# Kernel tuning notes

Measured on AMD Instinct MI355X. Metric: run time of the kernel, lower is better.

Reference implementation:

```python
import jax, jax.numpy as jnp
import numpy as np

N, H, C, G = 50000, 16, 8, 128   # nodes, heads, per-head channels, graphs
F_IN, NUM_CLASSES = 128, 2
E = 800000
HC = H * C
NEG_SLOPE = 0.2
BN_EPS = 1e-5


def setup_inputs() -> dict:
    key = jax.random.key(0)
    ks = jax.random.split(key, 32)
    s = 0.1
    p = lambda k, shape: (jax.random.normal(k, shape, jnp.float32) * s)
    inp = {
        "x": jax.random.normal(ks[0], (N, F_IN), jnp.float32),
        "edge_index": jax.random.randint(ks[1], (2, E), 0, N, dtype=jnp.int32),
        "batch": jnp.sort(jax.random.randint(ks[2], (N,), 0, G, dtype=jnp.int32)),
        # GAT layer 1 (in=F_IN)
        "W1": p(ks[3], (F_IN, HC)), "b1": p(ks[4], (HC,)),
        "asrc1": p(ks[5], (H, C)), "adst1": p(ks[6], (H, C)),
        "g1": 1.0 + p(ks[7], (HC,)), "beta1": p(ks[8], (HC,)),
        # GAT layer 2 (in=HC)
        "W2": p(ks[9], (HC, HC)), "b2": p(ks[10], (HC,)),
        "asrc2": p(ks[11], (H, C)), "adst2": p(ks[12], (H, C)),
        "g2": 1.0 + p(ks[13], (HC,)), "beta2": p(ks[14], (HC,)),
        # GAT layer 3
        "W3": p(ks[15], (HC, HC)), "b3": p(ks[16], (HC,)),
        "asrc3": p(ks[17], (H, C)), "adst3": p(ks[18], (H, C)),
        "g3": 1.0 + p(ks[19], (HC,)), "beta3": p(ks[20], (HC,)),
        # final linear + bn4
        "Wl": p(ks[21], (2 * HC, NUM_CLASSES)), "bl": p(ks[22], (NUM_CLASSES,)),
        "g4": 1.0 + p(ks[23], (NUM_CLASSES,)), "beta4": p(ks[24], (NUM_CLASSES,)),
    }
    return inp


def _gat(x, src, dst, W, b, asrc, adst):
    # x: [N, F_in] -> h: [N, H, C]
    h = (x @ W).reshape(N, H, C)
    a_s = jnp.einsum("nhc,hc->nh", h, asrc)  # [N,H]
    a_d = jnp.einsum("nhc,hc->nh", h, adst)
    e = jax.nn.leaky_relu(a_s[src] + a_d[dst], NEG_SLOPE)  # [E',H]
    # per-destination softmax (every node has a self loop -> segments non-empty)
    e_max = jax.ops.segment_max(e, dst, num_segments=N)
    ex = jnp.exp(e - e_max[dst])
    denom = jax.ops.segment_sum(ex, dst, num_segments=N)
    alpha = ex / (denom[dst] + 1e-16)  # [E',H]
    out = jax.ops.segment_sum(h[src] * alpha[:, :, None], dst, num_segments=N)
    return out.reshape(N, HC) + b


def _bn(x, g, beta):
    mu = jnp.mean(x, axis=0)
    var = jnp.mean((x - mu) ** 2, axis=0)  # biased, training-mode BN
    return (x - mu) * jax.lax.rsqrt(var + BN_EPS) * g + beta


def reference(x, edge_index, batch,
              W1, b1, asrc1, adst1, g1, beta1,
              W2, b2, asrc2, adst2, g2, beta2,
              W3, b3, asrc3, adst3, g3, beta3,
              Wl, bl, g4, beta4):
    # add self loops once (add_self_loops=True in every GATConv)
    loop = jnp.arange(N, dtype=edge_index.dtype)
    src = jnp.concatenate([edge_index[0], loop])
    dst = jnp.concatenate([edge_index[1], loop])

    h = jax.nn.relu(_bn(_gat(x, src, dst, W1, b1, asrc1, adst1), g1, beta1))
    h = jax.nn.relu(_bn(_gat(h, src, dst, W2, b2, asrc2, adst2), g2, beta2))
    h = jax.nn.relu(_bn(_gat(h, src, dst, W3, b3, asrc3, adst3), g3, beta3))

    pooled_sum = jax.ops.segment_sum(h, batch, num_segments=G)        # [G,HC]
    cnt = jax.ops.segment_sum(jnp.ones((N,), h.dtype), batch, num_segments=G)
    pooled_mean = pooled_sum / jnp.maximum(cnt, 1.0)[:, None]
    z = jnp.concatenate([pooled_mean, pooled_sum], axis=1)            # [G,2*HC]
    z = z @ Wl + bl
    return _bn(z, g4, beta4)
```

## Files before the change

kernel.cpp:

```cpp
#include <hip/hip_runtime.h>

#define NN 50000
#define NHEADS 16
#define NGRAPH 128
#define NEDGE 800000
#define NEP (NEDGE + NN)

#define EPB 2048
#define NBLK 416
#define NBUK 391
#define CASTB 3125
#define WTB 192
#define WASB 48

typedef float4 f4;
typedef __attribute__((ext_vector_type(4))) float f32x4;
typedef __attribute__((ext_vector_type(8))) short s8;

__device__ inline unsigned short f2b(float f) {
  union { float f; unsigned u; } v; v.f = f;
  unsigned r = v.u + 0x7FFFu + ((v.u >> 16) & 1u);
  return (unsigned short)(r >> 16);
}
__device__ inline float b2f(unsigned u16) {
  union { unsigned u; float f; } v; v.u = u16 << 16;
  return v.f;
}
__device__ inline float blo(unsigned u) {
  union { unsigned u; float f; } v; v.u = u << 16;
  return v.f;
}
__device__ inline float bhi(unsigned u) {
  union { unsigned u; float f; } v; v.u = u & 0xffff0000u;
  return v.f;
}


__global__ __launch_bounds__(256) void k_front(const int* __restrict__ ei, int* __restrict__ cntmat,
                                               const float* __restrict__ X, unsigned short* __restrict__ Xb,
                                               const float* __restrict__ W0, const float* __restrict__ W1, const float* __restrict__ W2,
                                               const float* __restrict__ as0, const float* __restrict__ as1, const float* __restrict__ as2,
                                               const float* __restrict__ ad0, const float* __restrict__ ad1, const float* __restrict__ ad2,
                                               unsigned short* __restrict__ T0, unsigned short* __restrict__ T1, unsigned short* __restrict__ T2,
                                               const int* __restrict__ batch, int* __restrict__ gstart) {
  __shared__ int hist[NBUK];
  int b = blockIdx.x, t = threadIdx.x;
  if (b < NBLK) {
    for (int k = t; k < NBUK; k += 256) hist[k] = 0;
    __syncthreads();
    int i0 = b * EPB;
    int i1 = i0 + EPB < NEP ? i0 + EPB : NEP;
    for (int i = i0 + t; i < i1; i += 256) {
      int d = (i < NEDGE) ? ei[NEDGE + i] : (i - NEDGE);
      atomicAdd(&hist[d >> 7], 1);
    }
    __syncthreads();
    for (int k = t; k < NBUK; k += 256) cntmat[b * NBUK + k] = hist[k];
    return;
  }
  int pb = b - NBLK;
  if (pb < CASTB) {
    int i = pb * 256 + t;
    const f4* X4 = (const f4*)X;
    f4 a = X4[2 * i], c = X4[2 * i + 1];
    uint4 o;
    o.x = (unsigned)f2b(a.x) | ((unsigned)f2b(a.y) << 16);
    o.y = (unsigned)f2b(a.z) | ((unsigned)f2b(a.w) << 16);
    o.z = (unsigned)f2b(c.x) | ((unsigned)f2b(c.y) << 16);
    o.w = (unsigned)f2b(c.z) | ((unsigned)f2b(c.w) << 16);
    ((uint4*)Xb)[i] = o;
  } else if (pb < CASTB + WTB) {
    int idx = (pb - CASTB) * 256 + t;
    int L = idx >> 14, r = idx & 16383;
    int n = r >> 7, kk = r & 127;
    const float* W = (L == 0) ? W0 : (L == 1) ? W1 : W2;
    unsigned short* T = (L == 0) ? T0 : (L == 1) ? T1 : T2;
    T[n * 128 + kk] = f2b(W[kk * 128 + n]);
  } else if (pb < CASTB + WTB + WASB) {
    int idx = (pb - CASTB - WTB) * 256 + t;
    int L = idx >> 12, r = idx & 4095;
    int h2 = r >> 7, kk = r & 127;
    int h = h2 & 15;
    const float* W = (L == 0) ? W0 : (L == 1) ? W1 : W2;
    const float* av = (h2 < 16) ? ((L == 0) ? as0 : (L == 1) ? as1 : as2)
                                : ((L == 0) ? ad0 : (L == 1) ? ad1 : ad2);
    unsigned short* T = (L == 0) ? T0 : (L == 1) ? T1 : T2;
    float s = 0.f;
#pragma unroll
    for (int c = 0; c < 8; ++c) s += W[kk * 128 + h * 8 + c] * av[h * 8 + c];
    T[(128 + h2) * 128 + kk] = f2b(s);
  } else {
    int g = t;
    if (g > NGRAPH) return;
    int lo = 0, hi = NN;
    while (lo < hi) { int mid = (lo + hi) >> 1; if (batch[mid] < g) lo = mid + 1; else hi = mid; }
    gstart[g] = lo;
  }
}


__global__ __launch_bounds__(512) void k_bscan(int* __restrict__ cntmat, int* __restrict__ btotal) {
  __shared__ int buf[512];
  int t = threadIdx.x, k = blockIdx.x;
  int v = (t < NBLK) ? cntmat[t * NBUK + k] : 0;
  buf[t] = v;
  __syncthreads();
  for (int off = 1; off < 512; off <<= 1) {
    int y = (t >= off) ? buf[t - off] : 0;
    __syncthreads();
    buf[t] += y;
    __syncthreads();
  }
  if (t < NBLK) cntmat[t * NBUK + k] = buf[t] - v;
  if (t == 511) btotal[k] = buf[511];
}

__global__ __launch_bounds__(512) void k_bbase(const int* __restrict__ btotal, int* __restrict__ bbase) {
  __shared__ int buf[512];
  int t = threadIdx.x;
  int v = (t < NBUK) ? btotal[t] : 0;
  buf[t] = v;
  __syncthreads();
  for (int off = 1; off < 512; off <<= 1) {
    int y = (t >= off) ? buf[t - off] : 0;
    __syncthreads();
    buf[t] += y;
    __syncthreads();
  }
  if (t < NBUK) bbase[t] = buf[t] - v;
  if (t == 511) bbase[NBUK] = buf[511];
}

__global__ __launch_bounds__(256) void k_bscatter(const int* __restrict__ ei, const int* __restrict__ cntmat,
                                                  const int* __restrict__ bbase, unsigned* __restrict__ pairs) {
  __shared__ int cur[NBUK];
  int t = threadIdx.x, b = blockIdx.x;
  for (int k = t; k < NBUK; k += 256) cur[k] = bbase[k] + cntmat[b * NBUK + k];
  __syncthreads();
  int i0 = b * EPB;
  int i1 = i0 + EPB < NEP ? i0 + EPB : NEP;
  for (int i = i0 + t; i < i1; i += 256) {
    int s, d;
    if (i < NEDGE) { s = ei[i]; d = ei[NEDGE + i]; }
    else { s = d = i - NEDGE; }
    int pos = atomicAdd(&cur[d >> 7], 1);
    pairs[pos] = ((unsigned)(d & 127) << 16) | (unsigned)s;
  }
}

__global__ __launch_bounds__(256) void k_bfinal(const unsigned* __restrict__ pairs, const int* __restrict__ bbase,
                                                int* __restrict__ row_off, int* __restrict__ colp) {
  __shared__ int cnt[128];
  __shared__ int buf[128];
  __shared__ int cur[128];
  int t = threadIdx.x, k = blockIdx.x;
  int n0 = k << 7;
  if (t < 128) cnt[t] = 0;
  __syncthreads();
  int p0 = bbase[k], p1 = bbase[k + 1];
  for (int i = p0 + t; i < p1; i += 256) atomicAdd(&cnt[pairs[i] >> 16], 1);
  __syncthreads();
  if (t < 128) buf[t] = cnt[t];
  __syncthreads();
  for (int off = 1; off < 128; off <<= 1) {
    int y = (t < 128 && t >= off) ? buf[t - off] : 0;
    __syncthreads();
    if (t < 128) buf[t] += y;
    __syncthreads();
  }
  if (t < 128) {
    int excl = buf[t] - cnt[t];
    cur[t] = p0 + excl;
    if (n0 + t < NN) row_off[n0 + t] = p0 + excl;
  }
  if (k == NBUK - 1 && t == 0) row_off[NN] = p1;
  __syncthreads();
  for (int i = p0 + t; i < p1; i += 256) {
    unsigned r = pairs[i];
    int pos = atomicAdd(&cur[r >> 16], 1);
    colp[pos] = (int)(r & 0xffffu);
  }
}


template<int FUSE>
__global__ __launch_bounds__(256) void k_gemm_t(const unsigned short* __restrict__ A, const unsigned short* __restrict__ Wt,
                                                const float* __restrict__ sc, unsigned short* __restrict__ Hb,
                                                unsigned short* __restrict__ Asb, float* __restrict__ Ad) {
  int w = threadIdx.x >> 6, l = threadIdx.x & 63;
  int r0 = blockIdx.x * 128 + w * 32;
  int lr = l & 15, lg = l >> 4;
  f32x4 acc[2][10];
#pragma unroll
  for (int m = 0; m < 2; ++m)
#pragma unroll
    for (int n = 0; n < 10; ++n) acc[m][n] = (f32x4){0.f, 0.f, 0.f, 0.f};

#pragma unroll
  for (int ks = 0; ks < 4; ++ks) {
    int koff = ks * 32 + lg * 8;
    s8 a[2];
    if constexpr (FUSE) {
      f4 s0 = *(const f4*)(sc + koff),       s1 = *(const f4*)(sc + koff + 4);
      f4 h0 = *(const f4*)(sc + 128 + koff), h1 = *(const f4*)(sc + 128 + koff + 4);
#pragma unroll
      for (int m = 0; m < 2; ++m) {
        int row = r0 + m * 16 + lr;
        row = (row < NN) ? row : (NN - 1);
        uint4 raw = *(const uint4*)(A + (size_t)row * 128 + koff);
        float v0 = fmaxf(blo(raw.x) * s0.x + h0.x, 0.f);
        float v1 = fmaxf(bhi(raw.x) * s0.y + h0.y, 0.f);
        float v2 = fmaxf(blo(raw.y) * s0.z + h0.z, 0.f);
        float v3 = fmaxf(bhi(raw.y) * s0.w + h0.w, 0.f);
        float v4 = fmaxf(blo(raw.z) * s1.x + h1.x, 0.f);
        float v5 = fmaxf(bhi(raw.z) * s1.y + h1.y, 0.f);
        float v6 = fmaxf(blo(raw.w) * s1.z + h1.z, 0.f);
        float v7 = fmaxf(bhi(raw.w) * s1.w + h1.w, 0.f);
        union { s8 v; uint4 u; } pk;
        pk.u.x = (unsigned)f2b(v0) | ((unsigned)f2b(v1) << 16);
        pk.u.y = (unsigned)f2b(v2) | ((unsigned)f2b(v3) << 16);
        pk.u.z = (unsigned)f2b(v4) | ((unsigned)f2b(v5) << 16);
        pk.u.w = (unsigned)f2b(v6) | ((unsigned)f2b(v7) << 16);
        a[m] = pk.v;
      }
    } else {
#pragma unroll
      for (int m = 0; m < 2; ++m) {
        int row = r0 + m * 16 + lr;
        row = (row < NN) ? row : (NN - 1);
        a[m] = *(const s8*)(A + (size_t)row * 128 + koff);
      }
    }
#pragma unroll
    for (int n = 0; n < 10; ++n) {
      s8 b = *(const s8*)(Wt + (size_t)(n * 16 + lr) * 128 + koff);
#pragma unroll
      for (int m = 0; m < 2; ++m)
        acc[m][n] = __builtin_amdgcn_mfma_f32_16x16x32_bf16(a[m], b, acc[m][n], 0, 0, 0);
    }
  }

#pragma unroll
  for (int m = 0; m < 2; ++m) {
    int rowb = r0 + m * 16 + lg * 4;
#pragma unroll
    for (int n = 0; n < 8; ++n) {
      int colb = n * 16 + lr;
#pragma unroll
      for (int reg = 0; reg < 4; ++reg) {
        int row = rowb + reg;
        if (row < NN) Hb[(size_t)row * 128 + colb] = f2b(acc[m][n][reg]);
      }
    }
#pragma unroll
    for (int reg = 0; reg < 4; ++reg) {
      int row = rowb + reg;
      if (row < NN) {
        Asb[row * 16 + lr] = f2b(acc[m][8][reg]);
        Ad[row * 16 + lr] = acc[m][9][reg];
      }
    }
  }
}


__global__ __launch_bounds__(256, 4) void k_agg(const unsigned short* __restrict__ Hb, const unsigned short* __restrict__ Asb,
                                                const float* __restrict__ Ad,
                                                const int* __restrict__ row_off, const int* __restrict__ col,
                                                unsigned short* __restrict__ Vb) {
  int b = blockIdx.x;
  int half = (b >> 2) & 1;
  int nb = (b >> 3) * 4 + (b & 3);
  if (nb >= 3125) return;
  int t = threadIdx.x;
  int node = nb * 16 + (t >> 4);
  int l = t & 15;
  int h = half * 8 + (l & 7);
  int par = l >> 3;
  int e0 = row_off[node], e1 = row_off[node + 1];
  float adh = Ad[node * 16 + h];
  float den = 0.f;
  float acc[8] = {0.f, 0.f, 0.f, 0.f, 0.f, 0.f, 0.f, 0.f};
  int j = e0 + par;
  for (; j + 14 < e1; j += 16) {
    int s[8];
#pragma unroll
    for (int q = 0; q < 8; ++q) s[q] = col[j + 2 * q];
    float a[8];
#pragma unroll
    for (int q = 0; q < 8; ++q) a[q] = b2f(Asb[s[q] * 16 + h]);
    uint4 p[8];
#pragma unroll
    for (int q = 0; q < 8; ++q) p[q] = *(const uint4*)(Hb + (size_t)s[q] * 128 + h * 8);
#pragma unroll
    for (int q = 0; q < 8; ++q) {
      float e = a[q] + adh;
      e = (e > 0.f) ? e : 0.2f * e;
      a[q] = __expf(e);
      den += a[q];
    }
#pragma unroll
    for (int q = 0; q < 8; ++q) {
      acc[0] += a[q] * blo(p[q].x); acc[1] += a[q] * bhi(p[q].x);
      acc[2] += a[q] * blo(p[q].y); acc[3] += a[q] * bhi(p[q].y);
      acc[4] += a[q] * blo(p[q].z); acc[5] += a[q] * bhi(p[q].z);
      acc[6] += a[q] * blo(p[q].w); acc[7] += a[q] * bhi(p[q].w);
    }
  }
  for (; j + 6 < e1; j += 8) {
    int s[4];
#pragma unroll
    for (int q = 0; q < 4; ++q) s[q] = col[j + 2 * q];
    float a[4];
#pragma unroll
    for (int q = 0; q < 4; ++q) a[q] = b2f(Asb[s[q] * 16 + h]);
    uint4 p[4];
#pragma unroll
    for (int q = 0; q < 4; ++q) p[q] = *(const uint4*)(Hb + (size_t)s[q] * 128 + h * 8);
#pragma unroll
    for (int q = 0; q < 4; ++q) {
      float e = a[q] + adh;
      e = (e > 0.f) ? e : 0.2f * e;
      a[q] = __expf(e);
      den += a[q];
    }
#pragma unroll
    for (int q = 0; q < 4; ++q) {
      acc[0] += a[q] * blo(p[q].x); acc[1] += a[q] * bhi(p[q].x);
      acc[2] += a[q] * blo(p[q].y); acc[3] += a[q] * bhi(p[q].y);
      acc[4] += a[q] * blo(p[q].z); acc[5] += a[q] * bhi(p[q].z);
      acc[6] += a[q] * blo(p[q].w); acc[7] += a[q] * bhi(p[q].w);
    }
  }
  for (; j < e1; j += 2) {
    int s0 = col[j];
    float a0 = b2f(Asb[s0 * 16 + h]) + adh;
    uint4 p0 = *(const uint4*)(Hb + (size_t)s0 * 128 + h * 8);
    a0 = (a0 > 0.f) ? a0 : 0.2f * a0;
    float x0 = __expf(a0);
    den += x0;
    acc[0] += x0 * blo(p0.x); acc[1] += x0 * bhi(p0.x);
    acc[2] += x0 * blo(p0.y); acc[3] += x0 * bhi(p0.y);
    acc[4] += x0 * blo(p0.z); acc[5] += x0 * bhi(p0.z);
    acc[6] += x0 * blo(p0.w); acc[7] += x0 * bhi(p0.w);
  }
  den += __shfl_xor(den, 8);
#pragma unroll
  for (int k = 0; k < 8; ++k) acc[k] += __shfl_xor(acc[k], 8);
  if (par == 0) {
    float inv = 1.f / (den + 1e-16f);
    uint4 o;
    o.x = (unsigned)f2b(acc[0] * inv) | ((unsigned)f2b(acc[1] * inv) << 16);
    o.y = (unsigned)f2b(acc[2] * inv) | ((unsigned)f2b(acc[3] * inv) << 16);
    o.z = (unsigned)f2b(acc[4] * inv) | ((unsigned)f2b(acc[5] * inv) << 16);
    o.w = (unsigned)f2b(acc[6] * inv) | ((unsigned)f2b(acc[7] * inv) << 16);
    *(uint4*)(Vb + (size_t)node * 128 + h * 8) = o;
  }
}


#define BN_CHUNK 391

__global__ __launch_bounds__(256) void k_bnreduce(const unsigned short* __restrict__ Vb, float* __restrict__ partS, float* __restrict__ partQ) {
  int t = threadIdx.x;
  int c4 = t & 31, rs = t >> 5;
  int r0 = blockIdx.x * BN_CHUNK + rs;
  int rend = blockIdx.x * BN_CHUNK + BN_CHUNK;
  if (rend > NN) rend = NN;
  float s0 = 0.f, s1 = 0.f, s2 = 0.f, s3 = 0.f;
  float q0 = 0.f, q1 = 0.f, q2 = 0.f, q3 = 0.f;
  for (int r = r0; r < rend; r += 8) {
    uint2 p = *(const uint2*)(Vb + (size_t)r * 128 + c4 * 4);
    float v0 = blo(p.x), v1 = bhi(p.x);
    float v2 = blo(p.y), v3 = bhi(p.y);
    s0 += v0; s1 += v1; s2 += v2; s3 += v3;
    q0 += v0 * v0; q1 += v1 * v1; q2 += v2 * v2; q3 += v3 * v3;
  }
  __shared__ float sm[8][32][8];
  sm[rs][c4][0] = s0; sm[rs][c4][1] = s1; sm[rs][c4][2] = s2; sm[rs][c4][3] = s3;
  sm[rs][c4][4] = q0; sm[rs][c4][5] = q1; sm[rs][c4][6] = q2; sm[rs][c4][7] = q3;
  __syncthreads();
  if (t < 32) {
#pragma unroll
    for (int k = 0; k < 4; ++k) {
      float S = 0.f, Q = 0.f;
#pragma unroll
      for (int r = 0; r < 8; ++r) { S += sm[r][t][k]; Q += sm[r][t][4 + k]; }
      partS[blockIdx.x * 128 + t * 4 + k] = S;
      partQ[blockIdx.x * 128 + t * 4 + k] = Q;
    }
  }
}

__global__ __launch_bounds__(512) void k_bnfin(const float* __restrict__ partS, const float* __restrict__ partQ,
                                               const float* __restrict__ gam, const float* __restrict__ bet,
                                               float* __restrict__ sc) {
  int t = threadIdx.x;
  int c = t & 127, q = (t >> 7) & 1, hf = t >> 8;
  const float* src = q ? partQ : partS;
  float s = 0.f;
#pragma unroll 8
  for (int i = hf * 64; i < hf * 64 + 64; ++i) s += src[i * 128 + c];
  __shared__ float sm[512];
  sm[t] = s;
  __syncthreads();
  if (t < 128) {
    float S = sm[t] + sm[t + 256];
    float Q = sm[t + 128] + sm[t + 384];
    float mean = S * (1.f / NN);
    float var = fmaxf(Q * (1.f / NN) - mean * mean, 0.f);
    float sg = gam[t] * rsqrtf(var + 1e-5f);
    sc[t] = sg;
    sc[128 + t] = bet[t] - mean * sg;
  }
}


__global__ __launch_bounds__(256) void k_pool(const unsigned short* __restrict__ Vb, const float* __restrict__ sc,
                                              const int* __restrict__ gstart, float* __restrict__ pp) {
  int g = blockIdx.x >> 2, chunk = blockIdx.x & 3;
  int t = threadIdx.x;
  int c4 = t & 31, rs = t >> 5;
  f4 s = ((const f4*)sc)[c4], sh = ((const f4*)sc)[32 + c4];
  int r0 = gstart[g], r1 = gstart[g + 1];
  float s0 = 0.f, s1 = 0.f, s2 = 0.f, s3 = 0.f;
  for (int r = r0 + chunk + 4 * rs; r < r1; r += 32) {
    uint2 p = *(const uint2*)(Vb + (size_t)r * 128 + c4 * 4);
    s0 += fmaxf(blo(p.x) * s.x + sh.x, 0.f);
    s1 += fmaxf(bhi(p.x) * s.y + sh.y, 0.f);
    s2 += fmaxf(blo(p.y) * s.z + sh.z, 0.f);
    s3 += fmaxf(bhi(p.y) * s.w + sh.w, 0.f);
  }
  __shared__ float sm[8][32][4];
  sm[rs][c4][0] = s0; sm[rs][c4][1] = s1; sm[rs][c4][2] = s2; sm[rs][c4][3] = s3;
  __syncthreads();
  if (t < 32) {
#pragma unroll
    for (int k = 0; k < 4; ++k) {
      float S = 0.f;
#pragma unroll
      for (int r = 0; r < 8; ++r) S += sm[r][t][k];
      pp[(size_t)blockIdx.x * 128 + t * 4 + k] = S;
    }
  }
}

__global__ __launch_bounds__(256) void k_final(const float* __restrict__ pp, const int* __restrict__ gstart,
                                               const float* __restrict__ Wl, const float* __restrict__ bl,
                                               const float* __restrict__ g4, const float* __restrict__ b4,
                                               float* __restrict__ out) {
  int t = threadIdx.x;
  int g = t >> 1, cls = t & 1;
  float cnt = fmaxf((float)(gstart[g + 1] - gstart[g]), 1.f);
  float inv = 1.f / cnt;
  float z = bl[cls];
  for (int f = 0; f < 128; ++f) {
    float ps = pp[(size_t)(g * 4 + 0) * 128 + f] + pp[(size_t)(g * 4 + 1) * 128 + f]
             + pp[(size_t)(g * 4 + 2) * 128 + f] + pp[(size_t)(g * 4 + 3) * 128 + f];
    z += ps * inv * Wl[f * 2 + cls] + ps * Wl[(128 + f) * 2 + cls];
  }
  __shared__ float zs[256];
  __shared__ float st[4];
  zs[t] = z;
  __syncthreads();
  if (t < 2) {
    float s = 0.f, s2 = 0.f;
    for (int gg = 0; gg < 128; ++gg) { float v = zs[gg * 2 + t]; s += v; s2 += v * v; }
    float mean = s * (1.f / 128.f);
    float var = s2 * (1.f / 128.f) - mean * mean;
    var = fmaxf(var, 0.f);
    float sc = g4[t] * rsqrtf(var + 1e-5f);
    st[t] = sc; st[2 + t] = b4[t] - mean * sc;
  }
  __syncthreads();
  out[t] = zs[t] * st[cls] + st[2 + cls];
}


extern "C" void kernel_launch(void* const* d_in, const int* in_sizes, int n_in,
                              void* d_out, int out_size, void* d_ws, size_t ws_size,
                              hipStream_t stream) {
  const float* x     = (const float*)d_in[0];
  const int*   ei    = (const int*)d_in[1];
  const int*   batch = (const int*)d_in[2];
  const float* W[3]    = {(const float*)d_in[3],  (const float*)d_in[9],  (const float*)d_in[15]};
  const float* asrc[3] = {(const float*)d_in[5],  (const float*)d_in[11], (const float*)d_in[17]};
  const float* adst[3] = {(const float*)d_in[6],  (const float*)d_in[12], (const float*)d_in[18]};
  const float* gam[3]  = {(const float*)d_in[7],  (const float*)d_in[13], (const float*)d_in[19]};
  const float* bet[3]  = {(const float*)d_in[8],  (const float*)d_in[14], (const float*)d_in[20]};
  const float* Wl    = (const float*)d_in[21];
  const float* bl    = (const float*)d_in[22];
  const float* g4    = (const float*)d_in[23];
  const float* beta4 = (const float*)d_in[24];

  char* ws = (char*)d_ws;
  size_t off = 0;
  auto alloc = [&](size_t bytes) -> void* {
    void* p = (void*)(ws + off);
    off += (bytes + 255) & ~(size_t)255;
    return p;
  };

  int* row_off  = (int*)alloc((size_t)(NN + 1) * 4);
  int* col      = (int*)alloc((size_t)NEP * 4);
  int* cntmat   = (int*)alloc((size_t)NBLK * NBUK * 4);
  int* btotal   = (int*)alloc((size_t)NBUK * 4);
  int* bbase    = (int*)alloc((size_t)(NBUK + 1) * 4);
  unsigned* pairs = (unsigned*)alloc((size_t)NEP * 4);
  unsigned short* Xb = (unsigned short*)alloc((size_t)NN * 128 * 2);
  unsigned short* Hb = (unsigned short*)alloc((size_t)NN * 128 * 2);
  unsigned short* Vb = (unsigned short*)alloc((size_t)NN * 128 * 2);
  unsigned short* Asb = (unsigned short*)alloc((size_t)NN * 16 * 2);
  float* Ad     = (float*)alloc((size_t)NN * 16 * 4);
  unsigned short* Wt0 = (unsigned short*)alloc((size_t)160 * 128 * 2);
  unsigned short* Wt1 = (unsigned short*)alloc((size_t)160 * 128 * 2);
  unsigned short* Wt2 = (unsigned short*)alloc((size_t)160 * 128 * 2);
  const unsigned short* Wt[3] = {Wt0, Wt1, Wt2};
  float* partS  = (float*)alloc(128 * 128 * 4);
  float* partQ  = (float*)alloc(128 * 128 * 4);
  float* bn_sc  = (float*)alloc(256 * 4);
  float* pp     = (float*)alloc((size_t)NGRAPH * 4 * 128 * 4);
  int* gstart   = (int*)alloc((size_t)(NGRAPH + 1) * 4);

  k_front<<<NBLK + CASTB + WTB + WASB + 1, 256, 0, stream>>>(ei, cntmat, x, Xb, W[0], W[1], W[2],
                                                             asrc[0], asrc[1], asrc[2], adst[0], adst[1], adst[2],
                                                             Wt0, Wt1, Wt2, batch, gstart);
  k_bscan<<<NBUK, 512, 0, stream>>>(cntmat, btotal);
  k_bbase<<<1, 512, 0, stream>>>(btotal, bbase);
  k_bscatter<<<NBLK, 256, 0, stream>>>(ei, cntmat, bbase, pairs);
  k_bfinal<<<NBUK, 256, 0, stream>>>(pairs, bbase, row_off, col);

  for (int L = 0; L < 3; ++L) {
    if (L == 0)
      k_gemm_t<0><<<(NN + 127) / 128, 256, 0, stream>>>(Xb, Wt[L], nullptr, Hb, Asb, Ad);
    else
      k_gemm_t<1><<<(NN + 127) / 128, 256, 0, stream>>>(Vb, Wt[L], bn_sc, Hb, Asb, Ad);
    k_agg<<<6256, 256, 0, stream>>>(Hb, Asb, Ad, row_off, col, Vb);
    k_bnreduce<<<128, 256, 0, stream>>>(Vb, partS, partQ);
    k_bnfin<<<1, 512, 0, stream>>>(partS, partQ, gam[L], bet[L], bn_sc);
  }

  k_pool<<<NGRAPH * 4, 256, 0, stream>>>(Vb, bn_sc, gstart, pp);
  k_final<<<1, 256, 0, stream>>>(pp, gstart, Wl, bl, g4, beta4, (float*)d_out);
}
```

Before: 282.2 us.

## Split node features into per-quarter-head planes for cache-local aggregation gathers

The GEMM now writes H and the source attention scores into four column-quarter planes (each 4 heads, 32 channels per node), and each aggregation block handles one quarter for 32 nodes. Gathers from neighbour rows then touch a 64-byte slice inside a compact plane instead of 128-byte rows across the whole array, which improves L2 locality per block. The GEMM tile is also halved from 128 to 64 rows per block, which doubles the block count but lowers per-thread accumulator pressure. The trade-off is scattered 64-byte output writes from the GEMM and a block ordering that may run all quarters of a node group concurrently.

Result: slower. 322.4 us (+14.2%).

```diff
diff --git a/kernel.cpp b/kernel.cpp
--- a/kernel.cpp
+++ b/kernel.cpp
@@ -185,98 +185,87 @@
 
 template<int FUSE>
 __global__ __launch_bounds__(256) void k_gemm_t(const unsigned short* __restrict__ A, const unsigned short* __restrict__ Wt,
-                                                const float* __restrict__ sc, unsigned short* __restrict__ Hb,
-                                                unsigned short* __restrict__ Asb, float* __restrict__ Ad) {
+                                                const float* __restrict__ sc, unsigned short* __restrict__ Hq,
+                                                unsigned short* __restrict__ Asq, float* __restrict__ Ad) {
   int w = threadIdx.x >> 6, l = threadIdx.x & 63;
-  int r0 = blockIdx.x * 128 + w * 32;
+  int r0 = blockIdx.x * 64 + w * 16;
   int lr = l & 15, lg = l >> 4;
-  f32x4 acc[2][10];
-#pragma unroll
-  for (int m = 0; m < 2; ++m)
-#pragma unroll
-    for (int n = 0; n < 10; ++n) acc[m][n] = (f32x4){0.f, 0.f, 0.f, 0.f};
+  f32x4 acc[10];
+#pragma unroll
+  for (int n = 0; n < 10; ++n) acc[n] = (f32x4){0.f, 0.f, 0.f, 0.f};
 
 #pragma unroll
   for (int ks = 0; ks < 4; ++ks) {
     int koff = ks * 32 + lg * 8;
-    s8 a[2];
+    s8 a;
+    int row = r0 + lr;
+    row = (row < NN) ? row : (NN - 1);
     if constexpr (FUSE) {
       f4 s0 = *(const f4*)(sc + koff),       s1 = *(const f4*)(sc + koff + 4);
       f4 h0 = *(const f4*)(sc + 128 + koff), h1 = *(const f4*)(sc + 128 + koff + 4);
-#pragma unroll
-      for (int m = 0; m < 2; ++m) {
-        int row = r0 + m * 16 + lr;
-        row = (row < NN) ? row : (NN - 1);
-        uint4 raw = *(const uint4*)(A + (size_t)row * 128 + koff);
-        float v0 = fmaxf(blo(raw.x) * s0.x + h0.x, 0.f);
-        float v1 = fmaxf(bhi(raw.x) * s0.y + h0.y, 0.f);
-        float v2 = fmaxf(blo(raw.y) * s0.z + h0.z, 0.f);
-        float v3 = fmaxf(bhi(raw.y) * s0.w + h0.w, 0.f);
-        float v4 = fmaxf(blo(raw.z) * s1.x + h1.x, 0.f);
-        float v5 = fmaxf(bhi(raw.z) * s1.y + h1.y, 0.f);
-        float v6 = fmaxf(blo(raw.w) * s1.z + h1.z, 0.f);
-        float v7 = fmaxf(bhi(raw.w) * s1.w + h1.w, 0.f);
-        union { s8 v; uint4 u; } pk;
-        pk.u.x = (unsigned)f2b(v0) | ((unsigned)f2b(v1) << 16);
-        pk.u.y = (unsigned)f2b(v2) | ((unsigned)f2b(v3) << 16);
-        pk.u.z = (unsigned)f2b(v4) | ((unsigned)f2b(v5) << 16);
-        pk.u.w = (unsigned)f2b(v6) | ((unsigned)f2b(v7) << 16);
-        a[m] = pk.v;
-      }
+      uint4 raw = *(const uint4*)(A + (size_t)row * 128 + koff);
+      float v0 = fmaxf(blo(raw.x) * s0.x + h0.x, 0.f);
+      float v1 = fmaxf(bhi(raw.x) * s0.y + h0.y, 0.f);
+      float v2 = fmaxf(blo(raw.y) * s0.z + h0.z, 0.f);
+      float v3 = fmaxf(bhi(raw.y) * s0.w + h0.w, 0.f);
+      float v4 = fmaxf(blo(raw.z) * s1.x + h1.x, 0.f);
+      float v5 = fmaxf(bhi(raw.z) * s1.y + h1.y, 0.f);
+      float v6 = fmaxf(blo(raw.w) * s1.z + h1.z, 0.f);
+      float v7 = fmaxf(bhi(raw.w) * s1.w + h1.w, 0.f);
+      union { s8 v; uint4 u; } pk;
+      pk.u.x = (unsigned)f2b(v0) | ((unsigned)f2b(v1) << 16);
+      pk.u.y = (unsigned)f2b(v2) | ((unsigned)f2b(v3) << 16);
+      pk.u.z = (unsigned)f2b(v4) | ((unsigned)f2b(v5) << 16);
+      pk.u.w = (unsigned)f2b(v6) | ((unsigned)f2b(v7) << 16);
+      a = pk.v;
     } else {
-#pragma unroll
-      for (int m = 0; m < 2; ++m) {
-        int row = r0 + m * 16 + lr;
-        row = (row < NN) ? row : (NN - 1);
-        a[m] = *(const s8*)(A + (size_t)row * 128 + koff);
-      }
+      a = *(const s8*)(A + (size_t)row * 128 + koff);
     }
 #pragma unroll
     for (int n = 0; n < 10; ++n) {
       s8 b = *(const s8*)(Wt + (size_t)(n * 16 + lr) * 128 + koff);
-#pragma unroll
-      for (int m = 0; m < 2; ++m)
-        acc[m][n] = __builtin_amdgcn_mfma_f32_16x16x32_bf16(a[m], b, acc[m][n], 0, 0, 0);
-    }
-  }
-
-#pragma unroll
-  for (int m = 0; m < 2; ++m) {
-    int rowb = r0 + m * 16 + lg * 4;
-#pragma unroll
-    for (int n = 0; n < 8; ++n) {
-      int colb = n * 16 + lr;
-#pragma unroll
-      for (int reg = 0; reg < 4; ++reg) {
-        int row = rowb + reg;
-        if (row < NN) Hb[(size_t)row * 128 + colb] = f2b(acc[m][n][reg]);
-      }
-    }
+      acc[n] = __builtin_amdgcn_mfma_f32_16x16x32_bf16(a, b, acc[n], 0, 0, 0);
+    }
+  }
+
+  int rowb = r0 + lg * 4;
+#pragma unroll
+  for (int n = 0; n < 8; ++n) {
+    int colb = n * 16 + lr;
+    int q = colb >> 5, cq = colb & 31;
 #pragma unroll
     for (int reg = 0; reg < 4; ++reg) {
       int row = rowb + reg;
-      if (row < NN) {
-        Asb[row * 16 + lr] = f2b(acc[m][8][reg]);
-        Ad[row * 16 + lr] = acc[m][9][reg];
-      }
-    }
-  }
-}
-
-
-__global__ __launch_bounds__(256, 4) void k_agg(const unsigned short* __restrict__ Hb, const unsigned short* __restrict__ Asb,
+      if (row < NN) Hq[(size_t)q * NN * 32 + (size_t)row * 32 + cq] = f2b(acc[n][reg]);
+    }
+  }
+  int hq = lr >> 2, hl = lr & 3;
+#pragma unroll
+  for (int reg = 0; reg < 4; ++reg) {
+    int row = rowb + reg;
+    if (row < NN) {
+      Asq[(size_t)hq * NN * 4 + (size_t)row * 4 + hl] = f2b(acc[8][reg]);
+      Ad[row * 16 + lr] = acc[9][reg];
+    }
+  }
+}
+
+
+__global__ __launch_bounds__(256, 4) void k_agg(const unsigned short* __restrict__ HqB, const unsigned short* __restrict__ AsqB,
                                                 const float* __restrict__ Ad,
                                                 const int* __restrict__ row_off, const int* __restrict__ col,
                                                 unsigned short* __restrict__ Vb) {
   int b = blockIdx.x;
-  int half = (b >> 2) & 1;
-  int nb = (b >> 3) * 4 + (b & 3);
-  if (nb >= 3125) return;
+  int q = (b & 7) >> 1;
+  int nb = (b >> 3) * 2 + (b & 1);
   int t = threadIdx.x;
-  int node = nb * 16 + (t >> 4);
-  int l = t & 15;
-  int h = half * 8 + (l & 7);
-  int par = l >> 3;
+  int node = nb * 32 + (t >> 3);
+  if (node >= NN) return;
+  const unsigned short* Hq = HqB + (size_t)q * NN * 32;
+  const unsigned short* Aq = AsqB + (size_t)q * NN * 4;
+  int l = t & 7;
+  int hl = l & 3, par = l >> 2;
+  int h = q * 4 + hl;
   int e0 = row_off[node], e1 = row_off[node + 1];
   float adh = Ad[node * 16 + h];
   float den = 0.f;
@@ -285,57 +274,57 @@
   for (; j + 14 < e1; j += 16) {
     int s[8];
 #pragma unroll
-    for (int q = 0; q < 8; ++q) s[q] = col[j + 2 * q];
+    for (int p = 0; p < 8; ++p) s[p] = col[j + 2 * p];
     float a[8];
 #pragma unroll
-    for (int q = 0; q < 8; ++q) a[q] = b2f(Asb[s[q] * 16 + h]);
-    uint4 p[8];
-#pragma unroll
-    for (int q = 0; q < 8; ++q) p[q] = *(const uint4*)(Hb + (size_t)s[q] * 128 + h * 8);
-#pragma unroll
-    for (int q = 0; q < 8; ++q) {
-      float e = a[q] + adh;
+    for (int p = 0; p < 8; ++p) a[p] = b2f(Aq[s[p] * 4 + hl]);
+    uint4 pp[8];
+#pragma unroll
+    for (int p = 0; p < 8; ++p) pp[p] = *(const uint4*)(Hq + (size_t)s[p] * 32 + hl * 8);
+#pragma unroll
+    for (int p = 0; p < 8; ++p) {
+      float e = a[p] + adh;
       e = (e > 0.f) ? e : 0.2f * e;
-      a[q] = __expf(e);
-      den += a[q];
-    }
-#pragma unroll
-    for (int q = 0; q < 8; ++q) {
-      acc[0] += a[q] * blo(p[q].x); acc[1] += a[q] * bhi(p[q].x);
-      acc[2] += a[q] * blo(p[q].y); acc[3] += a[q] * bhi(p[q].y);
-      acc[4] += a[q] * blo(p[q].z); acc[5] += a[q] * bhi(p[q].z);
-      acc[6] += a[q] * blo(p[q].w); acc[7] += a[q] * bhi(p[q].w);
+      a[p] = __expf(e);
+      den += a[p];
+    }
+#pragma unroll
+    for (int p = 0; p < 8; ++p) {
+      acc[0] += a[p] * blo(pp[p].x); acc[1] += a[p] * bhi(pp[p].x);
+      acc[2] += a[p] * blo(pp[p].y); acc[3] += a[p] * bhi(pp[p].y);
+      acc[4] += a[p] * blo(pp[p].z); acc[5] += a[p] * bhi(pp[p].z);
+      acc[6] += a[p] * blo(pp[p].w); acc[7] += a[p] * bhi(pp[p].w);
     }
   }
   for (; j + 6 < e1; j += 8) {
     int s[4];
 #pragma unroll
-    for (int q = 0; q < 4; ++q) s[q] = col[j + 2 * q];
+    for (int p = 0; p < 4; ++p) s[p] = col[j + 2 * p];
     float a[4];
 #pragma unroll
-    for (int q = 0; q < 4; ++q) a[q] = b2f(Asb[s[q] * 16 + h]);
-    uint4 p[4];
-#pragma unroll
-    for (int q = 0; q < 4; ++q) p[q] = *(const uint4*)(Hb + (size_t)s[q] * 128 + h * 8);
-#pragma unroll
-    for (int q = 0; q < 4; ++q) {
-      float e = a[q] + adh;
+    for (int p = 0; p < 4; ++p) a[p] = b2f(Aq[s[p] * 4 + hl]);
+    uint4 pp[4];
+#pragma unroll
+    for (int p = 0; p < 4; ++p) pp[p] = *(const uint4*)(Hq + (size_t)s[p] * 32 + hl * 8);
+#pragma unroll
+    for (int p = 0; p < 4; ++p) {
+      float e = a[p] + adh;
       e = (e > 0.f) ? e : 0.2f * e;
-      a[q] = __expf(e);
-      den += a[q];
-    }
-#pragma unroll
-    for (int q = 0; q < 4; ++q) {
-      acc[0] += a[q] * blo(p[q].x); acc[1] += a[q] * bhi(p[q].x);
-      acc[2] += a[q] * blo(p[q].y); acc[3] += a[q] * bhi(p[q].y);
-      acc[4] += a[q] * blo(p[q].z); acc[5] += a[q] * bhi(p[q].z);
-      acc[6] += a[q] * blo(p[q].w); acc[7] += a[q] * bhi(p[q].w);
+      a[p] = __expf(e);
+      den += a[p];
+    }
+#pragma unroll
+    for (int p = 0; p < 4; ++p) {
+      acc[0] += a[p] * blo(pp[p].x); acc[1] += a[p] * bhi(pp[p].x);
+      acc[2] += a[p] * blo(pp[p].y); acc[3] += a[p] * bhi(pp[p].y);
+      acc[4] += a[p] * blo(pp[p].z); acc[5] += a[p] * bhi(pp[p].z);
+      acc[6] += a[p] * blo(pp[p].w); acc[7] += a[p] * bhi(pp[p].w);
     }
   }
   for (; j < e1; j += 2) {
     int s0 = col[j];
-    float a0 = b2f(Asb[s0 * 16 + h]) + adh;
-    uint4 p0 = *(const uint4*)(Hb + (size_t)s0 * 128 + h * 8);
+    float a0 = b2f(Aq[s0 * 4 + hl]) + adh;
+    uint4 p0 = *(const uint4*)(Hq + (size_t)s0 * 32 + hl * 8);
     a0 = (a0 > 0.f) ? a0 : 0.2f * a0;
     float x0 = __expf(a0);
     den += x0;
@@ -344,9 +333,9 @@
     acc[4] += x0 * blo(p0.z); acc[5] += x0 * bhi(p0.z);
     acc[6] += x0 * blo(p0.w); acc[7] += x0 * bhi(p0.w);
   }
-  den += __shfl_xor(den, 8);
-#pragma unroll
-  for (int k = 0; k < 8; ++k) acc[k] += __shfl_xor(acc[k], 8);
+  den += __shfl_xor(den, 4);
+#pragma unroll
+  for (int k = 0; k < 8; ++k) acc[k] += __shfl_xor(acc[k], 4);
   if (par == 0) {
     float inv = 1.f / (den + 1e-16f);
     uint4 o;
@@ -354,7 +343,7 @@
     o.y = (unsigned)f2b(acc[2] * inv) | ((unsigned)f2b(acc[3] * inv) << 16);
     o.z = (unsigned)f2b(acc[4] * inv) | ((unsigned)f2b(acc[5] * inv) << 16);
     o.w = (unsigned)f2b(acc[6] * inv) | ((unsigned)f2b(acc[7] * inv) << 16);
-    *(uint4*)(Vb + (size_t)node * 128 + h * 8) = o;
+    *(uint4*)(Vb + (size_t)node * 128 + q * 32 + hl * 8) = o;
   }
 }
 
@@ -508,9 +497,9 @@
   int* bbase    = (int*)alloc((size_t)(NBUK + 1) * 4);
   unsigned* pairs = (unsigned*)alloc((size_t)NEP * 4);
   unsigned short* Xb = (unsigned short*)alloc((size_t)NN * 128 * 2);
-  unsigned short* Hb = (unsigned short*)alloc((size_t)NN * 128 * 2);
+  unsigned short* Hq = (unsigned short*)alloc((size_t)NN * 128 * 2);
   unsigned short* Vb = (unsigned short*)alloc((size_t)NN * 128 * 2);
-  unsigned short* Asb = (unsigned short*)alloc((size_t)NN * 16 * 2);
+  unsigned short* Asq = (unsigned short*)alloc((size_t)NN * 16 * 2);
   float* Ad     = (float*)alloc((size_t)NN * 16 * 4);
   unsigned short* Wt0 = (unsigned short*)alloc((size_t)160 * 128 * 2);
   unsigned short* Wt1 = (unsigned short*)alloc((size_t)160 * 128 * 2);
@@ -532,10 +521,10 @@
 
   for (int L = 0; L < 3; ++L) {
     if (L == 0)
-      k_gemm_t<0><<<(NN + 127) / 128, 256, 0, stream>>>(Xb, Wt[L], nullptr, Hb, Asb, Ad);
+      k_gemm_t<0><<<(NN + 63) / 64, 256, 0, stream>>>(Xb, Wt[L], nullptr, Hq, Asq, Ad);
     else
-      k_gemm_t<1><<<(NN + 127) / 128, 256, 0, stream>>>(Vb, Wt[L], bn_sc, Hb, Asb, Ad);
-    k_agg<<<6256, 256, 0, stream>>>(Hb, Asb, Ad, row_off, col, Vb);
+      k_gemm_t<1><<<(NN + 63) / 64, 256, 0, stream>>>(Vb, Wt[L], bn_sc, Hq, Asq, Ad);
+    k_agg<<<6256, 256, 0, stream>>>(Hq, Asq, Ad, row_off, col, Vb);
     k_bnreduce<<<128, 256, 0, stream>>>(Vb, partS, partQ);
     k_bnfin<<<1, 512, 0, stream>>>(partS, partQ, gam[L], bet[L], bn_sc);
   }
```
